# Kernel optimization log

Hardware: AMD Instinct MI355X
Metric: run time of the kernel (lower is better)

## Reference

```python
import math
import jax, jax.numpy as jnp
import numpy as np

S, M, B, NH, HD = 512, 512, 8, 16, 64  # SentenceLength, MemoryLength, BatchSize, heads, head_size
H = NH * HD   # 1024 hidden
K = M + S     # key length = r_length
LAYERS, TOTAL_LEN = 2, 1536


def setup_inputs() -> dict:
    key = jax.random.key(0)
    ks = jax.random.split(key, 12)
    w = lambda k: jax.random.normal(k, (H, H), jnp.float32) * 0.02
    return {
        "x": jax.random.normal(ks[0], (B, S, H), jnp.float32),
        "rel_pos_emb": jax.random.normal(ks[1], (K, H), jnp.float32),
        "attention_mask": jnp.ones((B, S), jnp.float32),  # unused by the original forward
        "memories": jax.random.normal(ks[2], (LAYERS, B, TOTAL_LEN, H), jnp.float32),
        "Wq": w(ks[3]), "Wke": w(ks[4]), "Wv": w(ks[5]), "Wkr": w(ks[6]),
        "u": jax.random.normal(ks[7], (NH, HD), jnp.float32),
        "v": jax.random.normal(ks[8], (NH, HD), jnp.float32),
        "Wo": w(ks[9]),
        "bo": jnp.zeros((H,), jnp.float32),
        "layer_num": 0,
        "segment_num": 0,
    }


def rel_shift(bd):
    # Vectorized form of the original per-row loop:
    # row qi keeps bd[qi][qlen-1-qi:] and zero-pads the tail.
    qlen, klen = bd.shape[0], bd.shape[1]
    shift = (qlen - 1) - jnp.arange(qlen)            # [qlen]
    idx = shift[:, None] + jnp.arange(klen)[None, :]  # [qlen, klen]
    valid = (idx < klen)
    idx_c = jnp.minimum(idx, klen - 1)
    out = bd[jnp.arange(qlen)[:, None], idx_c]        # gather along key axis
    return out * valid[:, :, None, None].astype(bd.dtype)


def reference(x, rel_pos_emb, attention_mask, memories, Wq, Wke, Wv, Wkr, u, v, Wo, bo, layer_num, segment_num):
    # memory segment for this layer: [B, M, H]
    sg_m = memories[layer_num, :, segment_num * M:(segment_num + 1) * M, :]
    kvx = jnp.concatenate([sg_m, x], axis=1)          # [B, K, H]
    # Projections, then the original's raw .view() reinterpretation (not a transpose)
    qx = (x.reshape(-1, H) @ Wq).reshape(S, B, NH, HD)
    kx = (kvx.reshape(-1, H) @ Wke).reshape(K, B, NH, HD)
    vx = (kvx.reshape(-1, H) @ Wv).reshape(K, B, NH, HD)
    kr = (rel_pos_emb @ Wkr).reshape(K, NH, HD)
    ac = jnp.einsum('ibnd,jbnd->ijbn', qx + u, kx)    # content score [S,K,B,NH]
    bd = jnp.einsum('ibnd,jnd->ijbn', qx + v, kr)     # position score
    bd = rel_shift(bd)
    att = (ac + bd) / math.sqrt(float(HD))
    att = jax.nn.softmax(att, axis=-1)                # original uses Softmax(dim=-1) on [i,j,b,n]
    out = jnp.einsum('ijbn,jbnd->ibnd', att, vx)      # [S,B,NH,HD]
    out = out.reshape(B, S, H)                        # original's raw contiguous().view()
    out = out @ Wo + bo                               # o_dense (dropout is identity in eval)
    # update_memories_by_layer (no_grad in torch -> stop_gradient here)
    new_mem = memories.at[layer_num, :, segment_num * S + M:(segment_num + 1) * S + M, :].set(
        jax.lax.stop_gradient(out))
    return out, new_mem
```

## Files before the change

kernel.cpp:

```cpp
#include <hip/hip_runtime.h>
#include <hip/hip_bf16.h>

#define OUT_OFF 4194304
#define NM_ELEMS 25165824

typedef __attribute__((ext_vector_type(8))) short short8;
typedef __attribute__((ext_vector_type(4))) float f32x4;

static __device__ __forceinline__ float4 ld4(const float* p) {
  return *reinterpret_cast<const float4*>(p);
}
static __device__ __forceinline__ short bfbits(float f) {
  __hip_bfloat16 h = __float2bfloat16(f);
  return *reinterpret_cast<short*>(&h);
}
static __device__ __forceinline__ void gload16(const void* g, void* l) {
  __builtin_amdgcn_global_load_lds(
      (const __attribute__((address_space(1))) void*)g,
      (__attribute__((address_space(3))) void*)l, 16, 0, 0);
}
static __device__ __forceinline__ void barrier_nodrain() {
  asm volatile("s_waitcnt lgkmcnt(0)" ::: "memory");
  __builtin_amdgcn_sched_barrier(0);
  __builtin_amdgcn_s_barrier();
  __builtin_amdgcn_sched_barrier(0);
}

__global__ __launch_bounds__(256)
void cw_k(const float* __restrict__ W0, const float* __restrict__ W1,
          const float* __restrict__ W2, const float* __restrict__ W3,
          const float* __restrict__ W4,
          __hip_bfloat16* __restrict__ T0, __hip_bfloat16* __restrict__ T1,
          __hip_bfloat16* __restrict__ T2, __hip_bfloat16* __restrict__ T3,
          __hip_bfloat16* __restrict__ T4)
{
  const float* W; __hip_bfloat16* T;
  switch (blockIdx.z) {
    case 0: W = W0; T = T0; break;
    case 1: W = W1; T = T1; break;
    case 2: W = W2; T = T2; break;
    case 3: W = W3; T = T3; break;
    default: W = W4; T = T4; break;
  }
  __shared__ short S[64][72];
  const int t = threadIdx.x;
  const int n0 = blockIdx.x * 64, k0 = blockIdx.y * 64;
  #pragma unroll
  for (int it = 0; it < 2; ++it) {
    const int kl = (t >> 3) + it * 32;
    const int n8 = (t & 7) * 8;
    const float* src = W + (size_t)(k0 + kl) * 1024 + n0 + n8;
    const float4 f0 = ld4(src), f1 = ld4(src + 4);
    short8 s;
    s[0]=bfbits(f0.x); s[1]=bfbits(f0.y); s[2]=bfbits(f0.z); s[3]=bfbits(f0.w);
    s[4]=bfbits(f1.x); s[5]=bfbits(f1.y); s[6]=bfbits(f1.z); s[7]=bfbits(f1.w);
    *reinterpret_cast<short8*>(&S[kl][n8]) = s;
  }
  __syncthreads();
  #pragma unroll
  for (int it = 0; it < 2; ++it) {
    const int nl = (t >> 3) + it * 32;
    const int k8 = (t & 7) * 8;
    short8 s;
    #pragma unroll
    for (int e = 0; e < 8; ++e) s[e] = S[k8 + e][nl];
    *reinterpret_cast<short8*>((short*)T + (size_t)(n0 + nl) * 1024 + k0 + k8) = s;
  }
}

__global__ __launch_bounds__(256)
void ckvx_k(const float* __restrict__ x, const float* __restrict__ mem,
            const int* __restrict__ lp, const int* __restrict__ sp,
            __hip_bfloat16* __restrict__ Kvx)
{
  const size_t t = (size_t)blockIdx.x * 256 + threadIdx.x;
  const int r = (int)(t >> 7);
  const int c = (int)(t & 127) * 8;
  const int b = r >> 10, j = r & 1023;
  const float* src = (j < 512)
    ? mem + (((size_t)lp[0] * 8 + b) * 1536 + (size_t)sp[0] * 512 + j) * 1024 + c
    : x + ((size_t)b * 512 + (j - 512)) * 1024 + c;
  const float4 f0 = ld4(src), f1 = ld4(src + 4);
  short8 s;
  s[0]=bfbits(f0.x); s[1]=bfbits(f0.y); s[2]=bfbits(f0.z); s[3]=bfbits(f0.w);
  s[4]=bfbits(f1.x); s[5]=bfbits(f1.y); s[6]=bfbits(f1.z); s[7]=bfbits(f1.w);
  *reinterpret_cast<short8*>((short*)Kvx + (size_t)r * 1024 + c) = s;
}

__global__ __launch_bounds__(256)
void crpe_k(const float* __restrict__ R, __hip_bfloat16* __restrict__ Rb)
{
  const size_t t = ((size_t)blockIdx.x * 256 + threadIdx.x) * 8;
  const float4 f0 = ld4(R + t), f1 = ld4(R + t + 4);
  short8 s;
  s[0]=bfbits(f0.x); s[1]=bfbits(f0.y); s[2]=bfbits(f0.z); s[3]=bfbits(f0.w);
  s[4]=bfbits(f1.x); s[5]=bfbits(f1.y); s[6]=bfbits(f1.z); s[7]=bfbits(f1.w);
  *reinterpret_cast<short8*>((short*)Rb + t) = s;
}

template<int MODE>
__global__ __launch_bounds__(256)
void mgemm(const __hip_bfloat16* __restrict__ A,
           const __hip_bfloat16* __restrict__ Wt,
           const float* __restrict__ P0, const float* __restrict__ P1,
           const int* __restrict__ lp, const int* __restrict__ sp,
           __hip_bfloat16* __restrict__ Cb, __hip_bfloat16* __restrict__ Cb2,
           float* __restrict__ C)
{
  __shared__ __align__(16) short As[128 * 64];
  __shared__ __align__(16) short Bs[128 * 64];
  const int tid = threadIdx.x;
  const int w   = tid >> 6;
  const int l   = tid & 63;
  const int l15 = l & 15, lg = l >> 4;
  const int m0 = blockIdx.y * 128;
  const int n0 = blockIdx.x * 128;
  const int wr = (w >> 1) * 64;
  const int wc = (w & 1) * 64;

  f32x4 acc[4][4];
  #pragma unroll
  for (int mi = 0; mi < 4; ++mi)
    #pragma unroll
    for (int ni = 0; ni < 4; ++ni) acc[mi][ni] = (f32x4){0.f, 0.f, 0.f, 0.f};

  const int srow = (l >> 3);
  const int scol = (l & 7) * 8;

  for (int k0 = 0; k0 < 1024; k0 += 64) {
    if (k0) __syncthreads();
    #pragma unroll
    for (int q = 0; q < 4; ++q) {
      const int seg = w * 32 + q * 8;
      const int ra = m0 + seg + srow;
      size_t aoff;
      if (MODE == 4)
        aoff = ((size_t)(ra >> 9) * 1024 + 512 + (ra & 511)) * 1024;
      else
        aoff = (size_t)ra * 1024;
      gload16((const short*)A + aoff + k0 + scol, &As[seg * 64]);
      const int rb = n0 + seg + srow;
      gload16((const short*)Wt + (size_t)rb * 1024 + k0 + scol, &Bs[seg * 64]);
    }
    __syncthreads();
    #pragma unroll
    for (int kk = 0; kk < 2; ++kk) {
      short8 a[4], bf[4];
      #pragma unroll
      for (int mi = 0; mi < 4; ++mi)
        a[mi] = *reinterpret_cast<const short8*>(
            &As[(wr + mi * 16 + l15) * 64 + kk * 32 + lg * 8]);
      #pragma unroll
      for (int ni = 0; ni < 4; ++ni)
        bf[ni] = *reinterpret_cast<const short8*>(
            &Bs[(wc + ni * 16 + l15) * 64 + kk * 32 + lg * 8]);
      #pragma unroll
      for (int mi = 0; mi < 4; ++mi)
        #pragma unroll
        for (int ni = 0; ni < 4; ++ni)
          acc[mi][ni] = __builtin_amdgcn_mfma_f32_16x16x32_bf16(
              a[mi], bf[ni], acc[mi][ni], 0, 0, 0);
    }
  }

  #pragma unroll
  for (int mi = 0; mi < 4; ++mi) {
    const int rbase = m0 + wr + mi * 16 + lg * 4;
    #pragma unroll
    for (int ni = 0; ni < 4; ++ni) {
      const int col = n0 + wc + ni * 16 + l15;
      #pragma unroll
      for (int rr = 0; rr < 4; ++rr) {
        const int row = rbase + rr;
        const float val = acc[mi][ni][rr];
        if (MODE == 3) {
          Cb[(size_t)row * 1024 + col] = __float2bfloat16(val);
        } else if (MODE == 4) {
          const int nh = col >> 6, dd = col & 63;
          const int i = row >> 3, bb = row & 7;
          const size_t o = (((size_t)(bb * 16 + nh) * 512) + i) * 64 + dd;
          Cb [o] = __float2bfloat16(val + P0[col]);
          Cb2[o] = __float2bfloat16(val + P1[col]);
        } else if (MODE == 7) {
          const int cc = col & 1023;
          const int nh = cc >> 6, dd = cc & 63;
          const int j = row >> 3, bb = row & 7;
          __hip_bfloat16* dst = (col < 1024) ? Cb : Cb2;
          dst[(((size_t)(bb * 16 + nh) * 1024) + j) * 64 + dd] =
              __float2bfloat16(val);
        } else if (MODE == 2) {
          const float o = val + P0[col];
          C[(size_t)row * 1024 + col] = o;
          const int b2 = row >> 9, s2 = row & 511;
          C[OUT_OFF +
            (((size_t)lp[0] * 8 + b2) * 1536 + 512 + (size_t)sp[0] * 512 + s2) *
                1024 + col] = o;
        }
      }
    }
  }
}

__global__ __launch_bounds__(256)
void tr_k(const __hip_bfloat16* __restrict__ VE, __hip_bfloat16* __restrict__ Vt)
{
  __shared__ short T[64][72];
  const int t = threadIdx.x;
  const int j0 = blockIdx.x * 64;
  const int bn = blockIdx.y;
  #pragma unroll
  for (int it = 0; it < 2; ++it) {
    const int jl = (t >> 3) + it * 32;
    const int d8 = (t & 7) * 8;
    *reinterpret_cast<short8*>(&T[jl][d8]) =
        *reinterpret_cast<const short8*>(
            (const short*)VE + ((size_t)bn * 1024 + j0 + jl) * 64 + d8);
  }
  __syncthreads();
  #pragma unroll
  for (int it = 0; it < 2; ++it) {
    const int dl = (t >> 3) + it * 32;
    const int j8 = (t & 7) * 8;
    short8 s;
    #pragma unroll
    for (int e = 0; e < 8; ++e) s[e] = T[j8 + e][dl];
    *reinterpret_cast<short8*>(
        (short*)Vt + ((size_t)bn * 64 + dl) * 1024 + j0 + j8) = s;
  }
}

__global__ __launch_bounds__(512, 1)
void attn2(const __hip_bfloat16* __restrict__ QU, const __hip_bfloat16* __restrict__ QV,
           const __hip_bfloat16* __restrict__ KE, const __hip_bfloat16* __restrict__ Vt,
           const __hip_bfloat16* __restrict__ KR, __hip_bfloat16* __restrict__ Ob)
{
  __shared__ __align__(16) short stg[49152];
  __shared__ float Lbuf[16*16*33];
  __shared__ __hip_bfloat16 Abuf[16*16*40];

  const int bid = blockIdx.x;
  const int b   = bid & 7;
  const int i0  = (bid >> 3) * 16;
  const int tid = threadIdx.x;
  const int w   = tid >> 6;
  const int l   = tid & 63;
  const int l15 = l & 15;
  const int lg  = l >> 4;

  short* keW = stg + w * 6144;
  short* krW = keW + 2048;

  const short* KEs = (const short*)KE;
  const short* KRs = (const short*)KR;

  short8 qu[2][2], qv[2][2];
  #pragma unroll
  for (int hh = 0; hh < 2; ++hh) {
    const int h = 2*w + hh;
    const size_t qb = (((size_t)(b*16 + h) * 512) + i0 + l15) * 64 + lg*8;
    #pragma unroll
    for (int kf = 0; kf < 2; ++kf) {
      qu[hh][kf] = *reinterpret_cast<const short8*>(QU + qb + kf*32);
      qv[hh][kf] = *reinterpret_cast<const short8*>(QV + qb + kf*32);
    }
  }

  f32x4 oacc[2][4];
  #pragma unroll
  for (int hh = 0; hh < 2; ++hh)
    #pragma unroll
    for (int nf = 0; nf < 4; ++nf) oacc[hh][nf] = (f32x4){0.f,0.f,0.f,0.f};

  auto stage = [&](int j0) {
    const int pb = 496 - i0 + j0;
    #pragma unroll
    for (int q = 0; q < 4; ++q) {
      const int R  = q*8 + (l >> 3);
      const int hh = R >> 4, jl = R & 15;
      const int c  = (l & 7) ^ (R & 7);
      gload16(KEs + (((size_t)(b*16 + 2*w + hh) * 1024) + j0 + jl) * 64 + c * 8,
              keW + q * 512);
    }
    #pragma unroll
    for (int q = 0; q < 8; ++q) {
      const int r = q*4 + (l >> 4);
      const int c = (l & 15) ^ (r & 15);
      gload16(KRs + ((size_t)(pb + r)) * 1024 + w * 128 + c * 8,
              krW + q * 512);
    }
  };

  stage(0);

  for (int pr = 0; pr < 32; ++pr) {
    const int j0e = pr * 32;
    short8 vb[2][4];

    #pragma unroll
    for (int half = 0; half < 2; ++half) {
      const int j0 = j0e + half * 16;

      asm volatile("s_waitcnt vmcnt(0)" ::: "memory");
      __builtin_amdgcn_sched_barrier(0);

      short8 kef[2][2], krf[2][2][2];
      #pragma unroll
      for (int hh = 0; hh < 2; ++hh)
        #pragma unroll
        for (int kf = 0; kf < 2; ++kf) {
          const int rowE = hh*16 + l15;
          const int kcE  = (kf*4 + lg) ^ (rowE & 7);
          kef[hh][kf] = *reinterpret_cast<const short8*>(
              keW + rowE*64 + kcE*8);
          #pragma unroll
          for (int nf = 0; nf < 2; ++nf) {
            const int rowR = nf*16 + l15;
            const int kcR  = (hh*8 + kf*4 + lg) ^ (rowR & 15);
            krf[hh][nf][kf] = *reinterpret_cast<const short8*>(
                krW + rowR*128 + kcR*8);
          }
        }

      __builtin_amdgcn_s_setprio(1);
      f32x4 ac[2], tf[2][2];
      #pragma unroll
      for (int hh = 0; hh < 2; ++hh) {
        ac[hh]    = (f32x4){0,0,0,0};
        tf[hh][0] = (f32x4){0,0,0,0};
        tf[hh][1] = (f32x4){0,0,0,0};
        #pragma unroll
        for (int kf = 0; kf < 2; ++kf) {
          ac[hh] = __builtin_amdgcn_mfma_f32_16x16x32_bf16(
              qu[hh][kf], kef[hh][kf], ac[hh], 0, 0, 0);
          #pragma unroll
          for (int nf = 0; nf < 2; ++nf)
            tf[hh][nf] = __builtin_amdgcn_mfma_f32_16x16x32_bf16(
                qv[hh][kf], krf[hh][nf][kf], tf[hh][nf], 0, 0, 0);
        }
      }
      __builtin_amdgcn_s_setprio(0);

      asm volatile("s_waitcnt lgkmcnt(0)" ::: "memory");
      __builtin_amdgcn_sched_barrier(0);
      stage(j0 + 16);
      if (half == 0) {
        #pragma unroll
        for (int hh = 0; hh < 2; ++hh) {
          const int h = 2*w + hh;
          #pragma unroll
          for (int nf = 0; nf < 4; ++nf)
            vb[hh][nf] = *reinterpret_cast<const short8*>(
              Vt + (((size_t)(b*16 + h) * 64) + nf*16 + l15) * 1024 + j0e + lg*8);
        }
      }

      #pragma unroll
      for (int hh = 0; hh < 2; ++hh) {
        const int h = 2*w + hh;
        #pragma unroll
        for (int r = 0; r < 4; ++r) {
          const int ip  = lg*4 + r;
          const int idx = 15 - ip + l15;
          const int nf  = idx >> 4;
          const int Ls  = lg*16 + (idx & 15);
          const float v0 = __shfl(tf[hh][0][r], Ls, 64);
          const float v1 = __shfl(tf[hh][1][r], Ls, 64);
          const float bd = nf ? v1 : v0;
          Lbuf[(h*16 + ip)*33 + half*16 + l15] = 0.125f * (ac[hh][r] + bd);
        }
      }
    }
    barrier_nodrain();

    {
      const int si = tid >> 5, sj = tid & 31;
      float vals[16];
      float m = -3.0e38f;
      #pragma unroll
      for (int n = 0; n < 16; ++n) {
        vals[n] = Lbuf[(n*16 + si)*33 + sj];
        m = fmaxf(m, vals[n]);
      }
      float s = 0.f;
      #pragma unroll
      for (int n = 0; n < 16; ++n) { vals[n] = __expf(vals[n] - m); s += vals[n]; }
      const float rinv = 1.0f / s;
      #pragma unroll
      for (int n = 0; n < 16; ++n)
        Abuf[(n*16 + si)*40 + sj] = __float2bfloat16(vals[n] * rinv);
    }
    barrier_nodrain();

    __builtin_amdgcn_s_setprio(1);
    #pragma unroll
    for (int hh = 0; hh < 2; ++hh) {
      const int h = 2*w + hh;
      const short8 af = *reinterpret_cast<const short8*>(
          &Abuf[(h*16 + l15)*40 + lg*8]);
      #pragma unroll
      for (int nf = 0; nf < 4; ++nf)
        oacc[hh][nf] = __builtin_amdgcn_mfma_f32_16x16x32_bf16(
            af, vb[hh][nf], oacc[hh][nf], 0, 0, 0);
    }
    __builtin_amdgcn_s_setprio(0);
  }

  #pragma unroll
  for (int hh = 0; hh < 2; ++hh) {
    const int h = 2*w + hh;
    #pragma unroll
    for (int nf = 0; nf < 4; ++nf)
      #pragma unroll
      for (int r = 0; r < 4; ++r) {
        const int i = i0 + lg*4 + r;
        Ob[((size_t)(i*8 + b)) * 1024 + h*64 + nf*16 + l15] =
            __float2bfloat16(oacc[hh][nf][r]);
      }
  }
}

extern "C" void kernel_launch(void* const* d_in, const int* in_sizes, int n_in,
                              void* d_out, int out_size, void* d_ws, size_t ws_size,
                              hipStream_t stream)
{
  const float* x   = (const float*)d_in[0];
  const float* rpe = (const float*)d_in[1];
  const float* mem = (const float*)d_in[3];
  const float* Wq  = (const float*)d_in[4];
  const float* Wke = (const float*)d_in[5];
  const float* Wv  = (const float*)d_in[6];
  const float* Wkr = (const float*)d_in[7];
  const float* u   = (const float*)d_in[8];
  const float* v   = (const float*)d_in[9];
  const float* Wo  = (const float*)d_in[10];
  const float* bo  = (const float*)d_in[11];
  const int* lp    = (const int*)d_in[12];
  const int* sp    = (const int*)d_in[13];

  float* out = (float*)d_out;
  float* nm  = out + OUT_OFF;

  float* ws = (float*)d_ws;
  __hip_bfloat16* QUb = (__hip_bfloat16*)(ws);
  __hip_bfloat16* QVb = (__hip_bfloat16*)(ws + 2097152);
  __hip_bfloat16* KRb = (__hip_bfloat16*)(ws + 4194304);
  __hip_bfloat16* Ob  = (__hip_bfloat16*)(ws + 4980736);
  __hip_bfloat16* Rb  = (__hip_bfloat16*)(ws + 7077888);
  __hip_bfloat16* WtO = (__hip_bfloat16*)(ws + 7602176);
  __hip_bfloat16* Kvx = (__hip_bfloat16*)(nm);
  __hip_bfloat16* KEb = (__hip_bfloat16*)(nm + 4194304);
  __hip_bfloat16* VEb = (__hip_bfloat16*)(nm + 8388608);
  __hip_bfloat16* Vtb = (__hip_bfloat16*)(nm + 12582912);
  __hip_bfloat16* WtQ = (__hip_bfloat16*)(nm + 16777216);
  __hip_bfloat16* WtK = (__hip_bfloat16*)(nm + 17301504);
  __hip_bfloat16* WtV = (__hip_bfloat16*)(nm + 17825792);
  __hip_bfloat16* WtR = (__hip_bfloat16*)(nm + 18350080);

  dim3 blk(256);
  hipMemsetAsync((void*)(KRb + (size_t)1024*1024), 0, (size_t)512*1024*2, stream);

  cw_k <<<dim3(16,16,5), blk, 0, stream>>>(Wq, Wke, Wv, Wkr, Wo,
                                           WtQ, WtK, WtV, WtR, WtO);
  ckvx_k<<<4096, blk, 0, stream>>>(x, mem, lp, sp, Kvx);
  crpe_k<<<512,  blk, 0, stream>>>(rpe, Rb);

  mgemm<3><<<dim3(8, 8),  blk, 0, stream>>>(Rb,  WtR, nullptr, nullptr, lp, sp, KRb, nullptr, nullptr);
  mgemm<4><<<dim3(8, 32), blk, 0, stream>>>(Kvx, WtQ, u, v,             lp, sp, QUb, QVb,     nullptr);
  mgemm<7><<<dim3(16, 64), blk, 0, stream>>>(Kvx, WtK, nullptr, nullptr, lp, sp, KEb, VEb, nullptr);

  tr_k<<<dim3(16, 128), blk, 0, stream>>>(VEb, Vtb);

  attn2<<<dim3(256), dim3(512), 0, stream>>>(QUb, QVb, KEb, Vtb, KRb, Ob);

  hipMemcpyAsync(nm, mem, (size_t)NM_ELEMS * 4ull, hipMemcpyDeviceToDevice, stream);

  mgemm<2><<<dim3(8, 32), blk, 0, stream>>>(Ob, WtO, bo, nullptr, lp, sp, nullptr, nullptr, out);
}
```

Baseline: 352.8 us.

## Fuse memory copy into output GEMM launch and remap blocks across XCDs

Drops the separate device-to-device memcpy of the full memories tensor. Extra z-slices of the final output GEMM grid now copy the rows instead, skipping the rows the GEMM output will overwrite, so copy and GEMM run concurrently. Block indices in all mgemm modes are also remapped so that consecutive hardware-dispatched blocks (round-robined across the 8 XCDs) share row tiles, aiming for better L2 locality. The copy traffic is about 100MB, so it likely dominates. The remap assumes GY is divisible by 8, which holds for these grids.

```diff
diff --git a/kernel.cpp b/kernel.cpp
--- a/kernel.cpp
+++ b/kernel.cpp
@@ -9,6 +9,9 @@
 
 static __device__ __forceinline__ float4 ld4(const float* p) {
   return *reinterpret_cast<const float4*>(p);
+}
+static __device__ __forceinline__ void st4(float* p, float4 v) {
+  *reinterpret_cast<float4*>(p) = v;
 }
 static __device__ __forceinline__ short bfbits(float f) {
   __hip_bfloat16 h = __float2bfloat16(f);
@@ -107,14 +110,41 @@
            __hip_bfloat16* __restrict__ Cb, __hip_bfloat16* __restrict__ Cb2,
            float* __restrict__ C)
 {
+  if (MODE == 2 && blockIdx.z > 0) {
+    const int cid = (int)((blockIdx.z - 1) * 256 + blockIdx.y * 8 + blockIdx.x);
+    const int layer = lp[0], seg = sp[0];
+    const int lo = 512 + seg * 512, hi = lo + 512;
+    float* nmp = C + OUT_OFF;
+    const float* src = P1;
+    const int t0 = threadIdx.x * 4;
+    const int r0 = cid * 48;
+    for (int r = r0; r < r0 + 48; ++r) {
+      const int t = r % 1536;
+      const int ly = r / (8 * 1536);
+      if (ly == layer && t >= lo && t < hi) continue;
+      st4(nmp + (size_t)r * 1024 + t0, ld4(src + (size_t)r * 1024 + t0));
+    }
+    return;
+  }
+
   __shared__ __align__(16) short As[128 * 64];
   __shared__ __align__(16) short Bs[128 * 64];
   const int tid = threadIdx.x;
   const int w   = tid >> 6;
   const int l   = tid & 63;
   const int l15 = l & 15, lg = l >> 4;
-  const int m0 = blockIdx.y * 128;
-  const int n0 = blockIdx.x * 128;
+
+  const int GX = gridDim.x, GY = gridDim.y;
+  int bx = blockIdx.x, by = blockIdx.y;
+  {
+    const int q   = by * GX + bx;
+    const int xcd = q & 7;
+    const int s   = q >> 3;
+    by = xcd * (GY >> 3) + s / GX;
+    bx = s % GX;
+  }
+  const int m0 = by * 128;
+  const int n0 = bx * 128;
   const int wr = (w >> 1) * 64;
   const int wc = (w & 1) * 64;
 
@@ -472,7 +502,5 @@
 
   attn2<<<dim3(256), dim3(512), 0, stream>>>(QUb, QVb, KEb, Vtb, KRb, Ob);
 
-  hipMemcpyAsync(nm, mem, (size_t)NM_ELEMS * 4ull, hipMemcpyDeviceToDevice, stream);
-
-  mgemm<2><<<dim3(8, 32), blk, 0, stream>>>(Ob, WtO, bo, nullptr, lp, sp, nullptr, nullptr, out);
-}
+  mgemm<2><<<dim3(8, 32, 3), blk, 0, stream>>>(Ob, WtO, bo, mem, lp, sp, nullptr, nullptr, out);
+}
```

Result: no change. 359.8 us (+2.0%).

## Fuse memories copy into attention kernel to overlap with compute

Applied to the files above, without the earlier changes.

The separate device-to-device memcpy of the memories tensor, about 100MB, is folded into the attention kernel. Each block streams one chunk per outer iteration through registers while the MFMA work runs, so the copy overlaps with the compute-bound attention instead of running as its own serialized pass. To do this, the KE and transposed-V scratch buffers move from the output region into the workspace when it is large enough, which avoids the copy overwriting buffers attention still reads. This adds register pressure and memory traffic inside attention, and it depends on the workspace size at runtime.

```diff
diff --git a/kernel.cpp b/kernel.cpp
--- a/kernel.cpp
+++ b/kernel.cpp
@@ -9,6 +9,9 @@
 
 static __device__ __forceinline__ float4 ld4(const float* p) {
   return *reinterpret_cast<const float4*>(p);
+}
+static __device__ __forceinline__ void st4(float* p, float4 v) {
+  *reinterpret_cast<float4*>(p) = v;
 }
 static __device__ __forceinline__ short bfbits(float f) {
   __hip_bfloat16 h = __float2bfloat16(f);
@@ -232,7 +235,8 @@
 __global__ __launch_bounds__(512, 1)
 void attn2(const __hip_bfloat16* __restrict__ QU, const __hip_bfloat16* __restrict__ QV,
            const __hip_bfloat16* __restrict__ KE, const __hip_bfloat16* __restrict__ Vt,
-           const __hip_bfloat16* __restrict__ KR, __hip_bfloat16* __restrict__ Ob)
+           const __hip_bfloat16* __restrict__ KR, __hip_bfloat16* __restrict__ Ob,
+           const float* __restrict__ Msrc, float* __restrict__ Mdst, int doCopy)
 {
   __shared__ __align__(16) short stg[49152];
   __shared__ float Lbuf[16*16*33];
@@ -271,6 +275,8 @@
     #pragma unroll
     for (int nf = 0; nf < 4; ++nf) oacc[hh][nf] = (f32x4){0.f,0.f,0.f,0.f};
 
+  float4 c0 = {0,0,0,0}, c1 = {0,0,0,0};
+
   auto stage = [&](int j0) {
     const int pb = 496 - i0 + j0;
     #pragma unroll
@@ -302,6 +308,21 @@
 
       asm volatile("s_waitcnt vmcnt(0)" ::: "memory");
       __builtin_amdgcn_sched_barrier(0);
+
+      if (half == 0 && doCopy) {
+        if (pr > 0) {
+          const size_t prev = (((size_t)((pr - 1) * 256 + bid)) * 512 + tid) * 8;
+          if (prev + 8 <= (size_t)NM_ELEMS) {
+            st4(Mdst + prev, c0);
+            st4(Mdst + prev + 4, c1);
+          }
+        }
+        const size_t cur = (((size_t)(pr * 256 + bid)) * 512 + tid) * 8;
+        if (cur + 8 <= (size_t)NM_ELEMS) {
+          c0 = ld4(Msrc + cur);
+          c1 = ld4(Msrc + cur + 4);
+        }
+      }
 
       short8 kef[2][2], krf[2][2][2];
       #pragma unroll
@@ -405,6 +426,14 @@
     __builtin_amdgcn_s_setprio(0);
   }
 
+  if (doCopy) {
+    const size_t last = (((size_t)(31 * 256 + bid)) * 512 + tid) * 8;
+    if (last + 8 <= (size_t)NM_ELEMS) {
+      st4(Mdst + last, c0);
+      st4(Mdst + last + 4, c1);
+    }
+  }
+
   #pragma unroll
   for (int hh = 0; hh < 2; ++hh) {
     const int h = 2*w + hh;
@@ -447,14 +476,18 @@
   __hip_bfloat16* Ob  = (__hip_bfloat16*)(ws + 4980736);
   __hip_bfloat16* Rb  = (__hip_bfloat16*)(ws + 7077888);
   __hip_bfloat16* WtO = (__hip_bfloat16*)(ws + 7602176);
+
+  const bool big = ws_size >= (size_t)16515072 * 4;
   __hip_bfloat16* Kvx = (__hip_bfloat16*)(nm);
-  __hip_bfloat16* KEb = (__hip_bfloat16*)(nm + 4194304);
   __hip_bfloat16* VEb = (__hip_bfloat16*)(nm + 8388608);
-  __hip_bfloat16* Vtb = (__hip_bfloat16*)(nm + 12582912);
   __hip_bfloat16* WtQ = (__hip_bfloat16*)(nm + 16777216);
   __hip_bfloat16* WtK = (__hip_bfloat16*)(nm + 17301504);
   __hip_bfloat16* WtV = (__hip_bfloat16*)(nm + 17825792);
   __hip_bfloat16* WtR = (__hip_bfloat16*)(nm + 18350080);
+  __hip_bfloat16* KEb = big ? (__hip_bfloat16*)(ws + 8126464)
+                            : (__hip_bfloat16*)(nm + 4194304);
+  __hip_bfloat16* Vtb = big ? (__hip_bfloat16*)(ws + 12320768)
+                            : (__hip_bfloat16*)(nm + 12582912);
 
   dim3 blk(256);
   hipMemsetAsync((void*)(KRb + (size_t)1024*1024), 0, (size_t)512*1024*2, stream);
@@ -470,9 +503,11 @@
 
   tr_k<<<dim3(16, 128), blk, 0, stream>>>(VEb, Vtb);
 
-  attn2<<<dim3(256), dim3(512), 0, stream>>>(QUb, QVb, KEb, Vtb, KRb, Ob);
-
-  hipMemcpyAsync(nm, mem, (size_t)NM_ELEMS * 4ull, hipMemcpyDeviceToDevice, stream);
+  attn2<<<dim3(256), dim3(512), 0, stream>>>(QUb, QVb, KEb, Vtb, KRb, Ob,
+                                             mem, nm, big ? 1 : 0);
+
+  if (!big)
+    hipMemcpyAsync(nm, mem, (size_t)NM_ELEMS * 4ull, hipMemcpyDeviceToDevice, stream);
 
   mgemm<2><<<dim3(8, 32), blk, 0, stream>>>(Ob, WtO, bo, nullptr, lp, sp, nullptr, nullptr, out);
 }
```

Result: faster. 338.4 us (-4.1%).
